# Performance work log

Measured on AMD Instinct MI355X. Metric: run time of the kernel, lower is better.

The kernel has to match this reference:

```python
import jax, jax.numpy as jnp
import numpy as np

H, DD, NCLS, NELEM, NPROP = 256, 32, 8, 11, 14
B, N = 4, 4096
ENC = NELEM + NPROP  # 25

_DIMS = [("dc1", ENC, H), ("dc21", H, DD), ("dc22", H, DD),
         ("in1", ENC, H), ("in2", H, H), ("in3", H, H),
         ("conv", H, H),
         ("id1", H, H), ("id2", H, H), ("id3", H, H),
         ("oid", H, NCLS), ("och", H, 2),
         ("m1", H + NCLS, H + NCLS), ("m2", H + NCLS, H), ("m3", H, H), ("om", H, 3)]


def setup_inputs() -> dict:
    key = jax.random.key(0)
    ks = jax.random.split(key, 2 + len(_DIMS))
    X = jax.random.normal(ks[0], (B, N, 15), jnp.float32)
    ids = jax.random.randint(ks[1], (B, N), 0, NELEM).astype(jnp.float32)
    X = X.at[:, :, 0].set(ids)
    d = {"X": X}
    for i, (name, di, do) in enumerate(_DIMS):
        W = jax.random.normal(ks[2 + i], (di, do), jnp.float32) / np.sqrt(di)
        d["W_" + name] = W
        d["b_" + name] = jnp.zeros((do,), jnp.float32)
    return d


def reference(X, W_dc1, b_dc1, W_dc21, b_dc21, W_dc22, b_dc22,
              W_in1, b_in1, W_in2, b_in2, W_in3, b_in3,
              W_conv, b_conv,
              W_id1, b_id1, W_id2, b_id2, W_id3, b_id3,
              W_oid, b_oid, W_och, b_och,
              W_m1, b_m1, W_m2, b_m2, W_m3, b_m3, W_om, b_om):
    act = jax.nn.selu
    # input encoding: one-hot element id (stop-grad via int cast) + properties, then selu
    onehot = jax.nn.one_hot(X[:, :, 0].astype(jnp.int32), NELEM, dtype=X.dtype)
    enc = act(jnp.concatenate([onehot, X[:, :, 1:]], axis=-1))  # [B,N,25]
    # distance coordinates
    h = act(enc @ W_dc1 + b_dc1)
    c1 = h @ W_dc21 + b_dc21  # [B,N,DD]
    c2 = h @ W_dc22 + b_dc22
    # pairwise distance -> exp adjacency
    na = jnp.sum(c1 * c1, -1)[:, :, None]
    nb = jnp.sum(c2 * c2, -1)[:, None, :]
    Dsq = jnp.clip(na - 2.0 * jnp.einsum('bnd,bmd->bnm', c1, c2) + nb, 1e-12, 1e12)
    adj = jnp.exp(-jnp.sqrt(Dsq))  # [B,N,N]
    # node MLP
    x = act(enc @ W_in1 + b_in1)
    x = act(x @ W_in2 + b_in2)
    x = act(x @ W_in3 + b_in3)
    # GraphConv: adj^k @ (x W) + b, k=4 (in-degree norm computed but unused upstream)
    x = act(jnp.einsum('bnm,bmh->bnh', adj ** 4, x @ W_conv) + b_conv)
    # id head
    a = act(x @ W_id1 + b_id1)
    a = act(a @ W_id2 + b_id2)
    a = act(a @ W_id3 + b_id3)
    out_id_logits = a @ W_oid + b_oid  # [B,N,8]
    out_charge = a @ W_och + b_och     # [B,N,2]
    # momentum head
    xb = jnp.concatenate([x, act(out_id_logits)], axis=-1)
    bb = act(xb @ W_m1 + b_m1)
    bb = act(bb @ W_m2 + b_m2)
    bb = act(bb @ W_m3 + b_m3)
    corr = bb @ W_om + b_om  # [B,N,3]
    mom = jnp.stack([X[:, :, 2] + corr[:, :, 0],
                     X[:, :, 3] + corr[:, :, 1],
                     X[:, :, 4] + corr[:, :, 2]], axis=-1)
    return jnp.concatenate([out_id_logits, mom, out_charge], axis=-1)  # [B,N,13]
```

## Files before the change

kernel.cpp:

```cpp
#include <hip/hip_runtime.h>
#include <cstddef>
#include <cstdint>

#define MROWS 16384
#define NSEQ  4096
#define ASTR  296
#define SELU_SCALE  1.0507009873554805f
#define SELU_ASCALE 1.7580993408473766f

typedef short bf16x8 __attribute__((ext_vector_type(8)));
typedef float f32x4  __attribute__((ext_vector_type(4)));

__device__ __forceinline__ float selu_f(float x) {
    return x > 0.f ? SELU_SCALE * x : SELU_ASCALE * (__expf(x) - 1.f);
}
__device__ __forceinline__ unsigned short f2bf(float x) {
    union { float f; unsigned int u; } v; v.f = x;
    unsigned int r = v.u + 0x7fffu + ((v.u >> 16) & 1u);
    return (unsigned short)(r >> 16);
}
__device__ __forceinline__ unsigned short t2bf(float x) {
    union { float f; unsigned int u; } v; v.f = x;
    return (unsigned short)(v.u >> 16);
}

struct PrepEnt { const float* W; unsigned short* WTf; int N, K, ntiles, KS, tileOff, tilesN; };
struct PrepArgs {
    PrepEnt e[16];
    const float *b21, *b22, *boid, *boch, *bdc1, *bin1;
    float *bc12, *boo, *bcat;
};
__global__ __launch_bounds__(256) void prep_kernel(PrepArgs pa) {
    if (blockIdx.y == 1) {
        if (blockIdx.x == 0) {
            int t = threadIdx.x;
            if (t < 32) pa.bc12[t] = pa.b21[t];
            else if (t < 64) pa.bc12[t] = pa.b22[t - 32];
            else if (t < 96) {
                int j = t - 64;
                pa.boo[j] = j < 8 ? pa.boid[j] : ((j >= 16 && j < 18) ? pa.boch[j - 16] : 0.f);
            }
        } else if (blockIdx.x == 1) {
            pa.bcat[threadIdx.x] = pa.bdc1[threadIdx.x];
        } else if (blockIdx.x == 2) {
            pa.bcat[256 + threadIdx.x] = pa.bin1[threadIdx.x];
        }
        return;
    }
    int bx = blockIdx.x;
    int ei = 0;
#pragma unroll
    for (int e = 1; e < 16; ++e)
        if (bx >= pa.e[e].tileOff) ei = e;
    PrepEnt E = pa.e[ei];
    int local = bx - E.tileOff;
    int tn = local / E.KS, tk = local - tn * E.KS;
    int k0 = tk * 32, n0 = tn * 32;

    __shared__ float ts[32][33];
    int t = threadIdx.x;
    {
        int kl = t >> 3, nl4 = (t & 7) * 4;
        int gk = k0 + kl;
#pragma unroll
        for (int j = 0; j < 4; ++j) {
            int gn = n0 + nl4 + j;
            float v = (gk < E.K && gn < E.N) ? E.W[(size_t)gk * E.N + gn] : 0.f;
            ts[nl4 + j][kl] = v;
        }
    }
    __syncthreads();
    int nl = t >> 3, kl4 = (t & 7) * 4;
    int n = n0 + nl;
    if (n < E.ntiles * 16) {
        ushort4 o;
        o.x = f2bf(ts[nl][kl4 + 0]);
        o.y = f2bf(ts[nl][kl4 + 1]);
        o.z = f2bf(ts[nl][kl4 + 2]);
        o.w = f2bf(ts[nl][kl4 + 3]);
        size_t dst = ((size_t)(n >> 4) * E.KS + tk) * 512 +
                     (size_t)((kl4 >> 3) * 16 + (n & 15)) * 8 + (kl4 & 7);
        *(ushort4*)(E.WTf + dst) = o;
    }
}

template <int MT, int NT>
__device__ __forceinline__ void zero_acc(f32x4 (&acc)[MT][NT]) {
#pragma unroll
    for (int i = 0; i < MT; ++i)
#pragma unroll
        for (int nt = 0; nt < NT; ++nt) acc[i][nt] = (f32x4){0.f, 0.f, 0.f, 0.f};
}

template <int MT, int NT, int K>
__device__ __forceinline__ void compute_tiles(
    f32x4 (&acc)[MT][NT],
    const unsigned short* __restrict__ src, int sstr,
    const unsigned short* __restrict__ WTf,
    int col0, int ln)
{
    constexpr int KS = (K + 31) / 32;
    int quad = ln >> 4, l15 = ln & 15;
    const unsigned short* wp = WTf + (size_t)(col0 >> 4) * (KS * 512) + ln * 8;
    bf16x8 bc[NT], bn[NT];
#pragma unroll
    for (int nt = 0; nt < NT; ++nt)
        bc[nt] = *(const bf16x8*)(wp + nt * (KS * 512));
    if (KS > 1) {
#pragma unroll
        for (int nt = 0; nt < NT; ++nt)
            bn[nt] = *(const bf16x8*)(wp + nt * (KS * 512) + 512);
    }
#pragma unroll
    for (int ks = 0; ks < KS; ++ks) {
        bf16x8 b2[NT];
        if (ks + 2 < KS) {
#pragma unroll
            for (int nt = 0; nt < NT; ++nt)
                b2[nt] = *(const bf16x8*)(wp + nt * (KS * 512) + (ks + 2) * 512);
        }
#pragma unroll
        for (int i = 0; i < MT; ++i) {
            bf16x8 af = *(const bf16x8*)(src + (i * 16 + l15) * sstr + ks * 32 + quad * 8);
#pragma unroll
            for (int nt = 0; nt < NT; ++nt)
                acc[i][nt] = __builtin_amdgcn_mfma_f32_16x16x32_bf16(af, bc[nt], acc[i][nt], 0, 0, 0);
        }
        if (ks + 1 < KS) {
#pragma unroll
            for (int nt = 0; nt < NT; ++nt) bc[nt] = bn[nt];
        }
        if (ks + 2 < KS) {
#pragma unroll
            for (int nt = 0; nt < NT; ++nt) bn[nt] = b2[nt];
        }
    }
}

template <int MT, int NT>
__device__ __forceinline__ void store_tiles(
    f32x4 (&acc)[MT][NT], unsigned short* __restrict__ dst,
    int col0, const float* __restrict__ bias, int Nreal, int act, int ln)
{
    int quad = ln >> 4, l15 = ln & 15;
#pragma unroll
    for (int nt = 0; nt < NT; ++nt) {
        int col = col0 + nt * 16 + l15;
        float bv = (bias && col < Nreal) ? bias[col] : 0.f;
#pragma unroll
        for (int i = 0; i < MT; ++i) {
#pragma unroll
            for (int r = 0; r < 4; ++r) {
                int row = i * 16 + quad * 4 + r;
                float v = acc[i][nt][r] + bv;
                if (act) v = selu_f(v);
                if (col >= Nreal) v = 0.f;
                dst[row * ASTR + col] = f2bf(v);
            }
        }
    }
}

__global__ __launch_bounds__(512) void pre_mega(
    const float* __restrict__ X,
    const unsigned short* __restrict__ WTdF, const float* __restrict__ bcat,
    const unsigned short* __restrict__ WTc12F, const float* __restrict__ bc12,
    const unsigned short* __restrict__ WTin2F, const float* __restrict__ b_in2,
    const unsigned short* __restrict__ WTin3F, const float* __restrict__ b_in3,
    const unsigned short* __restrict__ WTconvF,
    unsigned short* __restrict__ c1b, unsigned short* __restrict__ c2b,
    float* __restrict__ n1, float* __restrict__ n2,
    unsigned short* __restrict__ xwTb)
{
    __shared__ unsigned short encs[64 * 32];
    __shared__ unsigned short bufA[64 * ASTR];
    __shared__ unsigned short bufB[64 * ASTR];
    __shared__ float c12s[64 * 68];

    int tid = threadIdx.x, wv = tid >> 6, ln = tid & 63;
    int quad = ln >> 4, l15 = ln & 15;
    int row0 = blockIdx.x * 64;

#pragma unroll
    for (int p = 0; p < 4; ++p) {
        int idx = p * 512 + tid;
        int row = idx >> 5, col = idx & 31;
        float v = 0.f;
        if (col < 11) {
            int id = (int)X[(size_t)(row0 + row) * 15];
            v = (id == col) ? SELU_SCALE : 0.f;
        } else if (col < 25) {
            v = selu_f(X[(size_t)(row0 + row) * 15 + 1 + (col - 11)]);
        }
        encs[row * 32 + col] = f2bf(v);
    }
    __syncthreads();

#pragma unroll
    for (int ph = 0; ph < 2; ++ph) {
        f32x4 acc[4][2]; zero_acc<4, 2>(acc);
        compute_tiles<4, 2, 32>(acc, encs, 32, WTdF + (size_t)ph * 16 * 512, wv * 32, ln);
        store_tiles<4, 2>(acc, ph ? bufB : bufA, wv * 32, bcat + ph * 256, 256, 1, ln);
    }
    __syncthreads();

    if (wv < 2) {
        f32x4 acc[4][2]; zero_acc<4, 2>(acc);
        compute_tiles<4, 2, 256>(acc, bufA, ASTR, WTc12F, wv * 32, ln);
#pragma unroll
        for (int nt = 0; nt < 2; ++nt) {
            int col = wv * 32 + nt * 16 + l15;
            float bv = bc12[col];
#pragma unroll
            for (int i = 0; i < 4; ++i)
#pragma unroll
                for (int r = 0; r < 4; ++r)
                    c12s[(i * 16 + quad * 4 + r) * 68 + col] = acc[i][nt][r] + bv;
        }
    }
    __syncthreads();

    if (tid < 64) {
        int grow = row0 + tid;
        const float* p = &c12s[tid * 68];
        float s1 = 0.f, s2 = 0.f;
        unsigned int o1[16], o2[16];
#pragma unroll
        for (int k = 0; k < 32; k += 2) {
            float a0 = p[k], a1 = p[k + 1];
            s1 += a0 * a0 + a1 * a1;
            o1[k >> 1] = (unsigned)f2bf(a0) | ((unsigned)f2bf(a1) << 16);
            float b0 = p[32 + k], b1 = p[33 + k];
            s2 += b0 * b0 + b1 * b1;
            o2[k >> 1] = (unsigned)f2bf(b0) | ((unsigned)f2bf(b1) << 16);
        }
        uint4* d1 = (uint4*)(c1b + (size_t)grow * 32);
        uint4* d2 = (uint4*)(c2b + (size_t)grow * 32);
#pragma unroll
        for (int j = 0; j < 4; ++j) {
            d1[j] = make_uint4(o1[4 * j], o1[4 * j + 1], o1[4 * j + 2], o1[4 * j + 3]);
            d2[j] = make_uint4(o2[4 * j], o2[4 * j + 1], o2[4 * j + 2], o2[4 * j + 3]);
        }
        n1[grow] = s1;
        n2[grow] = s2;
    }

    {
        f32x4 acc[4][2]; zero_acc<4, 2>(acc);
        compute_tiles<4, 2, 256>(acc, bufB, ASTR, WTin2F, wv * 32, ln);
        store_tiles<4, 2>(acc, bufA, wv * 32, b_in2, 256, 1, ln);
    }
    __syncthreads();
    {
        f32x4 acc[4][2]; zero_acc<4, 2>(acc);
        compute_tiles<4, 2, 256>(acc, bufA, ASTR, WTin3F, wv * 32, ln);
        store_tiles<4, 2>(acc, bufB, wv * 32, b_in3, 256, 1, ln);
    }
    __syncthreads();
    {
        f32x4 acc[4][2]; zero_acc<4, 2>(acc);
        compute_tiles<4, 2, 256>(acc, bufB, ASTR, WTconvF, wv * 32, ln);
        store_tiles<4, 2>(acc, bufA, wv * 32, nullptr, 256, 0, ln);
    }
    __syncthreads();

    int b = row0 >> 12;
    int c0 = (row0 & 4095) >> 5;
#pragma unroll
    for (int p = 0; p < 4; ++p) {
        int idx = p * 512 + tid;
        int h = idx >> 3, mg = idx & 7;
        unsigned int w[4];
#pragma unroll
        for (int j = 0; j < 4; ++j) {
            unsigned int lo = bufA[(mg * 8 + 2 * j) * ASTR + h];
            unsigned int hi = bufA[(mg * 8 + 2 * j + 1) * ASTR + h];
            w[j] = lo | (hi << 16);
        }
        *(uint4*)(xwTb + ((size_t)((b * 128 + c0 + (mg >> 2)) * 256 + h) * 32) + (mg & 3) * 8) =
            make_uint4(w[0], w[1], w[2], w[3]);
    }
}

__global__ __launch_bounds__(512, 4) void adj_conv_mfma(
    const unsigned short* __restrict__ c1b, const unsigned short* __restrict__ c2b,
    const float* __restrict__ n1, const float* __restrict__ n2,
    const unsigned short* __restrict__ xwTb, const float* __restrict__ bconv,
    unsigned short* __restrict__ xc)
{
    __shared__ unsigned short wls[2][32][72];

    int tid = threadIdx.x, wv = tid >> 6, ln = tid & 63, quad = ln >> 4, l15 = ln & 15;
    int blk = blockIdx.x;
    int b = (blk >> 1) & 3;
    int iidx = ((blk >> 3) << 1) | (blk & 1);
    int i0 = iidx * 32;
    size_t base = (size_t)b * NSEQ;

    int it = wv & 1;
    int mt = wv >> 1;

    bf16x8 c1f = *(const bf16x8*)(c1b + (base + i0 + it * 16 + l15) * 32 + quad * 8);
    float4 n1v = *(const float4*)(n1 + base + i0 + it * 16 + quad * 4);

    const unsigned short* xwp0 = xwTb + (size_t)b * (128 * 256 * 32)
                               + ((size_t)(wv * 32 + l15) * 32 + quad * 8);
    const unsigned short* xwp1 = xwp0 + 8192;
    const unsigned short* c2p  = c2b + (base + mt * 16 + l15) * 32 + quad * 8;
    const float* n2p = n2 + base + mt * 16 + l15;

    f32x4 acc[2][2];
#pragma unroll
    for (int i = 0; i < 2; ++i)
#pragma unroll
        for (int j = 0; j < 2; ++j) acc[i][j] = (f32x4){0.f, 0.f, 0.f, 0.f};

    bf16x8 c2f = *(const bf16x8*)c2p;
    float nn2 = *n2p;
    bf16x8 bfc[2][2];
#pragma unroll
    for (int ht = 0; ht < 2; ++ht) {
        bfc[ht][0] = *(const bf16x8*)(xwp0 + ht * 512);
        bfc[ht][1] = *(const bf16x8*)(xwp1 + ht * 512);
    }
    xwp0 += 16384; xwp1 += 16384; c2p += 2048; n2p += 64;

#pragma unroll 2
    for (int itr = 0; itr < 64; ++itr) {
        int p = itr & 1;
        {
            f32x4 dotv = (f32x4){0.f, 0.f, 0.f, 0.f};
            dotv = __builtin_amdgcn_mfma_f32_16x16x32_bf16(c1f, c2f, dotv, 0, 0, 0);
#pragma unroll
            for (int r = 0; r < 4; ++r) {
                float D = fmaf(-2.f, dotv[r], n1v[r] + nn2);
                float t = __builtin_amdgcn_sqrtf(fmaxf(D, 1e-12f));
                wls[p][it * 16 + quad * 4 + r][mt * 16 + l15] = t2bf(__expf(t * -4.f));
            }
        }
        __syncthreads();

        bf16x8 af[2][2];
#pragma unroll
        for (int mi = 0; mi < 2; ++mi)
#pragma unroll
            for (int ks = 0; ks < 2; ++ks)
                af[mi][ks] = *(const bf16x8*)&wls[p][mi * 16 + l15][ks * 32 + quad * 8];

        bf16x8 bfn[2][2];
        if (itr < 63) {
            c2f = *(const bf16x8*)c2p;
            nn2 = *n2p;
#pragma unroll
            for (int ht = 0; ht < 2; ++ht) {
                bfn[ht][0] = *(const bf16x8*)(xwp0 + ht * 512);
                bfn[ht][1] = *(const bf16x8*)(xwp1 + ht * 512);
            }
            xwp0 += 16384; xwp1 += 16384; c2p += 2048; n2p += 64;
        }

#pragma unroll
        for (int mi = 0; mi < 2; ++mi)
#pragma unroll
            for (int ht = 0; ht < 2; ++ht)
#pragma unroll
                for (int ks = 0; ks < 2; ++ks)
                    acc[mi][ht] = __builtin_amdgcn_mfma_f32_16x16x32_bf16(
                        af[mi][ks], bfc[ht][ks], acc[mi][ht], 0, 0, 0);
        if (itr < 63) {
#pragma unroll
            for (int ht = 0; ht < 2; ++ht)
#pragma unroll
                for (int ks = 0; ks < 2; ++ks)
                    bfc[ht][ks] = bfn[ht][ks];
        }
    }

#pragma unroll
    for (int mi = 0; mi < 2; ++mi) {
#pragma unroll
        for (int ht = 0; ht < 2; ++ht) {
            int h = wv * 32 + ht * 16 + l15;
            float bv = bconv[h];
#pragma unroll
            for (int r = 0; r < 4; ++r) {
                int irow = i0 + mi * 16 + quad * 4 + r;
                xc[(base + irow) * 256 + h] = f2bf(selu_f(acc[mi][ht][r] + bv));
            }
        }
    }
}

__global__ __launch_bounds__(512) void post_mega(
    const float* __restrict__ X, const unsigned short* __restrict__ xc,
    const unsigned short* __restrict__ WTid1F, const float* __restrict__ b_id1,
    const unsigned short* __restrict__ WTid2F, const float* __restrict__ b_id2,
    const unsigned short* __restrict__ WTid3F, const float* __restrict__ b_id3,
    const unsigned short* __restrict__ WTooF, const float* __restrict__ boo,
    const unsigned short* __restrict__ WTm1F, const float* __restrict__ b_m1,
    const unsigned short* __restrict__ WTm2F, const float* __restrict__ b_m2,
    const unsigned short* __restrict__ WTm3F, const float* __restrict__ b_m3,
    const unsigned short* __restrict__ WTomF, const float* __restrict__ b_om,
    float* __restrict__ out)
{
    __shared__ unsigned short xcs[64 * ASTR];
    __shared__ unsigned short bufA[64 * ASTR];
    __shared__ unsigned short bufB[64 * ASTR];
    __shared__ float lgs[64 * 32];

    int tid = threadIdx.x, wv = tid >> 6, ln = tid & 63;
    int quad = ln >> 4, l15 = ln & 15;
    int row0 = blockIdx.x * 64;

#pragma unroll
    for (int p = 0; p < 4; ++p) {
        int idx = p * 512 + tid;
        int row = idx >> 5, c8 = (idx & 31) * 8;
        *(uint4*)&xcs[row * ASTR + c8] = *(const uint4*)(xc + (size_t)(row0 + row) * 256 + c8);
    }
#pragma unroll
    for (int p = 0; p < 5; ++p) {
        int idx = p * 512 + tid;
        int row = idx / 40, c = 256 + idx - row * 40;
        xcs[row * ASTR + c] = 0;
        bufB[row * ASTR + c] = 0;
    }
    __syncthreads();

    {
        f32x4 acc[4][2]; zero_acc<4, 2>(acc);
        compute_tiles<4, 2, 256>(acc, xcs, ASTR, WTid1F, wv * 32, ln);
        store_tiles<4, 2>(acc, bufA, wv * 32, b_id1, 256, 1, ln);
    }
    __syncthreads();
    {
        f32x4 acc[4][2]; zero_acc<4, 2>(acc);
        compute_tiles<4, 2, 256>(acc, bufA, ASTR, WTid2F, wv * 32, ln);
        store_tiles<4, 2>(acc, bufB, wv * 32, b_id2, 256, 1, ln);
    }
    __syncthreads();
    {
        f32x4 acc[4][2]; zero_acc<4, 2>(acc);
        compute_tiles<4, 2, 256>(acc, bufB, ASTR, WTid3F, wv * 32, ln);
        store_tiles<4, 2>(acc, bufA, wv * 32, b_id3, 256, 1, ln);
    }
    __syncthreads();
    if (wv == 0) {
        f32x4 acc[4][2]; zero_acc<4, 2>(acc);
        compute_tiles<4, 2, 256>(acc, bufA, ASTR, WTooF, 0, ln);
#pragma unroll
        for (int nt = 0; nt < 2; ++nt) {
            int col = nt * 16 + l15;
            float bv = boo[col];
#pragma unroll
            for (int i = 0; i < 4; ++i)
#pragma unroll
                for (int r = 0; r < 4; ++r)
                    lgs[(i * 16 + quad * 4 + r) * 32 + col] = acc[i][nt][r] + bv;
        }
    }
    __syncthreads();
    if (tid < 64) {
        float* op = out + (size_t)(row0 + tid) * 13;
#pragma unroll
        for (int c = 0; c < 8; ++c) {
            float lg = lgs[tid * 32 + c];
            op[c] = lg;
            xcs[tid * ASTR + 256 + c] = f2bf(selu_f(lg));
        }
        op[11] = lgs[tid * 32 + 16];
        op[12] = lgs[tid * 32 + 17];
    }
    __syncthreads();
    {
        f32x4 acc[4][2]; zero_acc<4, 2>(acc);
        compute_tiles<4, 2, 288>(acc, xcs, ASTR, WTm1F, wv * 32, ln);
        store_tiles<4, 2>(acc, bufB, wv * 32, b_m1, 264, 1, ln);
        if (wv == 0) {
            f32x4 acx[4][1]; zero_acc<4, 1>(acx);
            compute_tiles<4, 1, 288>(acx, xcs, ASTR, WTm1F, 256, ln);
            store_tiles<4, 1>(acx, bufB, 256, b_m1, 264, 1, ln);
        }
    }
    __syncthreads();
    {
        f32x4 acc[4][2]; zero_acc<4, 2>(acc);
        compute_tiles<4, 2, 288>(acc, bufB, ASTR, WTm2F, wv * 32, ln);
        store_tiles<4, 2>(acc, bufA, wv * 32, b_m2, 256, 1, ln);
    }
    __syncthreads();
    {
        f32x4 acc[4][2]; zero_acc<4, 2>(acc);
        compute_tiles<4, 2, 256>(acc, bufA, ASTR, WTm3F, wv * 32, ln);
        store_tiles<4, 2>(acc, bufB, wv * 32, b_m3, 256, 1, ln);
    }
    __syncthreads();
    if (wv == 0) {
        f32x4 acc[4][1]; zero_acc<4, 1>(acc);
        compute_tiles<4, 1, 256>(acc, bufB, ASTR, WTomF, 0, ln);
        if (l15 < 3) {
            float bv = b_om[l15];
#pragma unroll
            for (int i = 0; i < 4; ++i)
#pragma unroll
                for (int r = 0; r < 4; ++r) {
                    int grow = row0 + i * 16 + quad * 4 + r;
                    out[(size_t)grow * 13 + 8 + l15] =
                        X[(size_t)grow * 15 + 2 + l15] + acc[i][0][r] + bv;
                }
        }
    }
}

extern "C" void kernel_launch(void* const* d_in, const int* in_sizes, int n_in,
                              void* d_out, int out_size, void* d_ws, size_t ws_size,
                              hipStream_t stream) {
    (void)in_sizes; (void)n_in; (void)out_size; (void)ws_size;

    const float* X = (const float*)d_in[0];
    const float* W_dc1 = (const float*)d_in[1];  const float* b_dc1 = (const float*)d_in[2];
    const float* W_dc21 = (const float*)d_in[3]; const float* b_dc21 = (const float*)d_in[4];
    const float* W_dc22 = (const float*)d_in[5]; const float* b_dc22 = (const float*)d_in[6];
    const float* W_in1 = (const float*)d_in[7];  const float* b_in1 = (const float*)d_in[8];
    const float* W_in2 = (const float*)d_in[9];  const float* b_in2 = (const float*)d_in[10];
    const float* W_in3 = (const float*)d_in[11]; const float* b_in3 = (const float*)d_in[12];
    const float* W_conv = (const float*)d_in[13]; const float* b_conv = (const float*)d_in[14];
    const float* W_id1 = (const float*)d_in[15]; const float* b_id1 = (const float*)d_in[16];
    const float* W_id2 = (const float*)d_in[17]; const float* b_id2 = (const float*)d_in[18];
    const float* W_id3 = (const float*)d_in[19]; const float* b_id3 = (const float*)d_in[20];
    const float* W_oid = (const float*)d_in[21]; const float* b_oid = (const float*)d_in[22];
    const float* W_och = (const float*)d_in[23]; const float* b_och = (const float*)d_in[24];
    const float* W_m1 = (const float*)d_in[25];  const float* b_m1 = (const float*)d_in[26];
    const float* W_m2 = (const float*)d_in[27];  const float* b_m2 = (const float*)d_in[28];
    const float* W_m3 = (const float*)d_in[29];  const float* b_m3 = (const float*)d_in[30];
    const float* W_om = (const float*)d_in[31];  const float* b_om = (const float*)d_in[32];

    const size_t M = MROWS;
    char* pw = (char*)d_ws;
    auto alloc = [&](size_t bytes) -> void* {
        void* r = (void*)pw;
        pw += (bytes + 255) & ~(size_t)255;
        return r;
    };
    unsigned short* c1b = (unsigned short*)alloc(M * 32 * 2);
    unsigned short* c2b = (unsigned short*)alloc(M * 32 * 2);
    float* n1 = (float*)alloc(M * 4);
    float* n2 = (float*)alloc(M * 4);
    unsigned short* xwTb = (unsigned short*)alloc((size_t)4 * 128 * 256 * 32 * 2);
    unsigned short* xcb = (unsigned short*)alloc(M * 256 * 2);
    unsigned short* WTdF   = (unsigned short*)alloc((size_t)2 * 16 * 1 * 512 * 2);
    unsigned short* WTc12F = (unsigned short*)alloc((size_t)4 * 8 * 512 * 2);
    unsigned short* WTin2F = (unsigned short*)alloc((size_t)16 * 8 * 512 * 2);
    unsigned short* WTin3F = (unsigned short*)alloc((size_t)16 * 8 * 512 * 2);
    unsigned short* WTconvF = (unsigned short*)alloc((size_t)16 * 8 * 512 * 2);
    unsigned short* WTid1F = (unsigned short*)alloc((size_t)16 * 8 * 512 * 2);
    unsigned short* WTid2F = (unsigned short*)alloc((size_t)16 * 8 * 512 * 2);
    unsigned short* WTid3F = (unsigned short*)alloc((size_t)16 * 8 * 512 * 2);
    unsigned short* WTm3F  = (unsigned short*)alloc((size_t)16 * 8 * 512 * 2);
    unsigned short* WTooF  = (unsigned short*)alloc((size_t)2 * 8 * 512 * 2);
    unsigned short* WTm1F  = (unsigned short*)alloc((size_t)17 * 9 * 512 * 2);
    unsigned short* WTm2F  = (unsigned short*)alloc((size_t)16 * 9 * 512 * 2);
    unsigned short* WTomF  = (unsigned short*)alloc((size_t)1 * 8 * 512 * 2);
    float* bc12 = (float*)alloc(64 * 4);
    float* boo = (float*)alloc(32 * 4);
    float* bcat = (float*)alloc(512 * 4);

    PrepArgs pa;
    int off = 0;
    auto ent = [&](const float* W, unsigned short* WTf, int N, int K, int ntiles) {
        PrepEnt e; e.W = W; e.WTf = WTf; e.N = N; e.K = K; e.ntiles = ntiles;
        e.KS = (K + 31) / 32;
        e.tilesN = (ntiles * 16 + 31) / 32;
        e.tileOff = off;
        off += e.tilesN * e.KS;
        return e;
    };
    pa.e[0]  = ent(W_dc1,  WTdF,                256, 25,  16);
    pa.e[1]  = ent(W_in1,  WTdF + 16 * 512,     256, 25,  16);
    pa.e[2]  = ent(W_dc21, WTc12F,              32,  256, 2);
    pa.e[3]  = ent(W_dc22, WTc12F + 2 * 8 * 512, 32, 256, 2);
    pa.e[4]  = ent(W_in2,  WTin2F,              256, 256, 16);
    pa.e[5]  = ent(W_in3,  WTin3F,              256, 256, 16);
    pa.e[6]  = ent(W_conv, WTconvF,             256, 256, 16);
    pa.e[7]  = ent(W_id1,  WTid1F,              256, 256, 16);
    pa.e[8]  = ent(W_id2,  WTid2F,              256, 256, 16);
    pa.e[9]  = ent(W_id3,  WTid3F,              256, 256, 16);
    pa.e[10] = ent(W_m3,   WTm3F,               256, 256, 16);
    pa.e[11] = ent(W_oid,  WTooF,               8,   256, 1);
    pa.e[12] = ent(W_och,  WTooF + 8 * 512,     2,   256, 1);
    pa.e[13] = ent(W_m1,   WTm1F,               264, 264, 17);
    pa.e[14] = ent(W_m2,   WTm2F,               256, 264, 16);
    pa.e[15] = ent(W_om,   WTomF,               3,   256, 1);
    pa.b21 = b_dc21; pa.b22 = b_dc22; pa.boid = b_oid; pa.boch = b_och;
    pa.bdc1 = b_dc1; pa.bin1 = b_in1;
    pa.bc12 = bc12; pa.boo = boo; pa.bcat = bcat;
    prep_kernel<<<dim3(off, 2), 256, 0, stream>>>(pa);

    pre_mega<<<dim3(256), 512, 0, stream>>>(X, WTdF, bcat, WTc12F, bc12,
                                            WTin2F, b_in2, WTin3F, b_in3, WTconvF,
                                            c1b, c2b, n1, n2, xwTb);

    adj_conv_mfma<<<dim3(512), 512, 0, stream>>>(c1b, c2b, n1, n2, xwTb, b_conv, xcb);

    post_mega<<<dim3(256), 512, 0, stream>>>(X, xcb,
                                             WTid1F, b_id1, WTid2F, b_id2, WTid3F, b_id3,
                                             WTooF, boo, WTm1F, b_m1, WTm2F, b_m2,
                                             WTm3F, b_m3, WTomF, b_om, (float*)d_out);
}
```

Before: 261.9 us.

## Widen adjacency chunk to 128 columns per barrier and deepen weight prefetch

```diff
diff --git a/kernel.cpp b/kernel.cpp
--- a/kernel.cpp
+++ b/kernel.cpp
@@ -102,37 +102,33 @@
     constexpr int KS = (K + 31) / 32;
     int quad = ln >> 4, l15 = ln & 15;
     const unsigned short* wp = WTf + (size_t)(col0 >> 4) * (KS * 512) + ln * 8;
-    bf16x8 bc[NT], bn[NT];
-#pragma unroll
-    for (int nt = 0; nt < NT; ++nt)
-        bc[nt] = *(const bf16x8*)(wp + nt * (KS * 512));
-    if (KS > 1) {
-#pragma unroll
-        for (int nt = 0; nt < NT; ++nt)
-            bn[nt] = *(const bf16x8*)(wp + nt * (KS * 512) + 512);
+    bf16x8 st[3][NT];
+#pragma unroll
+    for (int s = 0; s < 3; ++s) {
+        if (s < KS) {
+#pragma unroll
+            for (int nt = 0; nt < NT; ++nt)
+                st[s][nt] = *(const bf16x8*)(wp + nt * (KS * 512) + s * 512);
+        }
     }
 #pragma unroll
     for (int ks = 0; ks < KS; ++ks) {
-        bf16x8 b2[NT];
-        if (ks + 2 < KS) {
+        bf16x8 bnew[NT];
+        if (ks + 3 < KS) {
 #pragma unroll
             for (int nt = 0; nt < NT; ++nt)
-                b2[nt] = *(const bf16x8*)(wp + nt * (KS * 512) + (ks + 2) * 512);
+                bnew[nt] = *(const bf16x8*)(wp + nt * (KS * 512) + (ks + 3) * 512);
         }
 #pragma unroll
         for (int i = 0; i < MT; ++i) {
             bf16x8 af = *(const bf16x8*)(src + (i * 16 + l15) * sstr + ks * 32 + quad * 8);
 #pragma unroll
             for (int nt = 0; nt < NT; ++nt)
-                acc[i][nt] = __builtin_amdgcn_mfma_f32_16x16x32_bf16(af, bc[nt], acc[i][nt], 0, 0, 0);
-        }
-        if (ks + 1 < KS) {
-#pragma unroll
-            for (int nt = 0; nt < NT; ++nt) bc[nt] = bn[nt];
-        }
-        if (ks + 2 < KS) {
-#pragma unroll
-            for (int nt = 0; nt < NT; ++nt) bn[nt] = b2[nt];
+                acc[i][nt] = __builtin_amdgcn_mfma_f32_16x16x32_bf16(af, st[ks % 3][nt], acc[i][nt], 0, 0, 0);
+        }
+        if (ks + 3 < KS) {
+#pragma unroll
+            for (int nt = 0; nt < NT; ++nt) st[ks % 3][nt] = bnew[nt];
         }
     }
 }
@@ -288,7 +284,7 @@
     const unsigned short* __restrict__ xwTb, const float* __restrict__ bconv,
     unsigned short* __restrict__ xc)
 {
-    __shared__ unsigned short wls[2][32][72];
+    __shared__ unsigned short wls[2][32][136];
 
     int tid = threadIdx.x, wv = tid >> 6, ln = tid & 63, quad = ln >> 4, l15 = ln & 15;
     int blk = blockIdx.x;
@@ -297,17 +293,18 @@
     int i0 = iidx * 32;
     size_t base = (size_t)b * NSEQ;
 
-    int it = wv & 1;
-    int mt = wv >> 1;
-
-    bf16x8 c1f = *(const bf16x8*)(c1b + (base + i0 + it * 16 + l15) * 32 + quad * 8);
-    float4 n1v = *(const float4*)(n1 + base + i0 + it * 16 + quad * 4);
+    bf16x8 c1f0 = *(const bf16x8*)(c1b + (base + i0 + l15) * 32 + quad * 8);
+    bf16x8 c1f1 = *(const bf16x8*)(c1b + (base + i0 + 16 + l15) * 32 + quad * 8);
+    float4 n1v0 = *(const float4*)(n1 + base + i0 + quad * 4);
+    float4 n1v1 = *(const float4*)(n1 + base + i0 + 16 + quad * 4);
 
     const unsigned short* xwp0 = xwTb + (size_t)b * (128 * 256 * 32)
                                + ((size_t)(wv * 32 + l15) * 32 + quad * 8);
     const unsigned short* xwp1 = xwp0 + 8192;
-    const unsigned short* c2p  = c2b + (base + mt * 16 + l15) * 32 + quad * 8;
-    const float* n2p = n2 + base + mt * 16 + l15;
+    const unsigned short* xwp2 = xwp0 + 16384;
+    const unsigned short* xwp3 = xwp0 + 24576;
+    const unsigned short* c2p  = c2b + (base + wv * 16 + l15) * 32 + quad * 8;
+    const float* n2p = n2 + base + wv * 16 + l15;
 
     f32x4 acc[2][2];
 #pragma unroll
@@ -317,62 +314,52 @@
 
     bf16x8 c2f = *(const bf16x8*)c2p;
     float nn2 = *n2p;
-    bf16x8 bfc[2][2];
-#pragma unroll
-    for (int ht = 0; ht < 2; ++ht) {
-        bfc[ht][0] = *(const bf16x8*)(xwp0 + ht * 512);
-        bfc[ht][1] = *(const bf16x8*)(xwp1 + ht * 512);
-    }
-    xwp0 += 16384; xwp1 += 16384; c2p += 2048; n2p += 64;
-
-#pragma unroll 2
-    for (int itr = 0; itr < 64; ++itr) {
+    c2p += 4096; n2p += 128;
+
+    for (int itr = 0; itr < 32; ++itr) {
         int p = itr & 1;
-        {
-            f32x4 dotv = (f32x4){0.f, 0.f, 0.f, 0.f};
-            dotv = __builtin_amdgcn_mfma_f32_16x16x32_bf16(c1f, c2f, dotv, 0, 0, 0);
-#pragma unroll
-            for (int r = 0; r < 4; ++r) {
-                float D = fmaf(-2.f, dotv[r], n1v[r] + nn2);
-                float t = __builtin_amdgcn_sqrtf(fmaxf(D, 1e-12f));
-                wls[p][it * 16 + quad * 4 + r][mt * 16 + l15] = t2bf(__expf(t * -4.f));
-            }
-        }
+        f32x4 d0 = (f32x4){0.f, 0.f, 0.f, 0.f};
+        f32x4 d1 = (f32x4){0.f, 0.f, 0.f, 0.f};
+        d0 = __builtin_amdgcn_mfma_f32_16x16x32_bf16(c1f0, c2f, d0, 0, 0, 0);
+        d1 = __builtin_amdgcn_mfma_f32_16x16x32_bf16(c1f1, c2f, d1, 0, 0, 0);
+        bf16x8 c2n; float nnn;
+        if (itr < 31) {
+            c2n = *(const bf16x8*)c2p;
+            nnn = *n2p;
+            c2p += 4096; n2p += 128;
+        }
+#pragma unroll
+        for (int r = 0; r < 4; ++r) {
+            float D0 = fmaf(-2.f, d0[r], n1v0[r] + nn2);
+            float D1 = fmaf(-2.f, d1[r], n1v1[r] + nn2);
+            float t0 = __builtin_amdgcn_sqrtf(fmaxf(D0, 1e-12f));
+            float t1 = __builtin_amdgcn_sqrtf(fmaxf(D1, 1e-12f));
+            wls[p][quad * 4 + r][wv * 16 + l15]      = t2bf(__expf(t0 * -4.f));
+            wls[p][16 + quad * 4 + r][wv * 16 + l15] = t2bf(__expf(t1 * -4.f));
+        }
+        if (itr < 31) { c2f = c2n; nn2 = nnn; }
         __syncthreads();
 
-        bf16x8 af[2][2];
-#pragma unroll
-        for (int mi = 0; mi < 2; ++mi)
-#pragma unroll
-            for (int ks = 0; ks < 2; ++ks)
-                af[mi][ks] = *(const bf16x8*)&wls[p][mi * 16 + l15][ks * 32 + quad * 8];
-
-        bf16x8 bfn[2][2];
-        if (itr < 63) {
-            c2f = *(const bf16x8*)c2p;
-            nn2 = *n2p;
-#pragma unroll
-            for (int ht = 0; ht < 2; ++ht) {
-                bfn[ht][0] = *(const bf16x8*)(xwp0 + ht * 512);
-                bfn[ht][1] = *(const bf16x8*)(xwp1 + ht * 512);
-            }
-            xwp0 += 16384; xwp1 += 16384; c2p += 2048; n2p += 64;
-        }
-
-#pragma unroll
-        for (int mi = 0; mi < 2; ++mi)
-#pragma unroll
-            for (int ht = 0; ht < 2; ++ht)
-#pragma unroll
-                for (int ks = 0; ks < 2; ++ks)
-                    acc[mi][ht] = __builtin_amdgcn_mfma_f32_16x16x32_bf16(
-                        af[mi][ks], bfc[ht][ks], acc[mi][ht], 0, 0, 0);
-        if (itr < 63) {
-#pragma unroll
-            for (int ht = 0; ht < 2; ++ht)
-#pragma unroll
-                for (int ks = 0; ks < 2; ++ks)
-                    bfc[ht][ks] = bfn[ht][ks];
+        bf16x8 bf0[2], bf1[2], bf2[2], bf3[2];
+#pragma unroll
+        for (int ht = 0; ht < 2; ++ht) {
+            bf0[ht] = *(const bf16x8*)(xwp0 + ht * 512);
+            bf1[ht] = *(const bf16x8*)(xwp1 + ht * 512);
+            bf2[ht] = *(const bf16x8*)(xwp2 + ht * 512);
+            bf3[ht] = *(const bf16x8*)(xwp3 + ht * 512);
+        }
+        xwp0 += 32768; xwp1 += 32768; xwp2 += 32768; xwp3 += 32768;
+
+#pragma unroll
+        for (int ks = 0; ks < 4; ++ks) {
+            bf16x8 af0 = *(const bf16x8*)&wls[p][l15][ks * 32 + quad * 8];
+            bf16x8 af1 = *(const bf16x8*)&wls[p][16 + l15][ks * 32 + quad * 8];
+            bf16x8 b0 = (ks == 0) ? bf0[0] : (ks == 1) ? bf1[0] : (ks == 2) ? bf2[0] : bf3[0];
+            bf16x8 b1 = (ks == 0) ? bf0[1] : (ks == 1) ? bf1[1] : (ks == 2) ? bf2[1] : bf3[1];
+            acc[0][0] = __builtin_amdgcn_mfma_f32_16x16x32_bf16(af0, b0, acc[0][0], 0, 0, 0);
+            acc[0][1] = __builtin_amdgcn_mfma_f32_16x16x32_bf16(af0, b1, acc[0][1], 0, 0, 0);
+            acc[1][0] = __builtin_amdgcn_mfma_f32_16x16x32_bf16(af1, b0, acc[1][0], 0, 0, 0);
+            acc[1][1] = __builtin_amdgcn_mfma_f32_16x16x32_bf16(af1, b1, acc[1][1], 0, 0, 0);
         }
     }
 
```

New measurement: 257.5 us. Within noise of the previous version (-1.7%).
